# Optimization experiments

Hardware: AMD Instinct MI355X
Metric: run time of the kernel (lower is better)

The kernel has to match this reference:

```python
import jax, jax.numpy as jnp
import numpy as np

B, S, D = 16, 2048, 768  # batch, padded subword length, roberta hidden dim


def setup_inputs() -> dict:
    key = jax.random.key(0)
    k1, k2 = jax.random.split(key)
    robert_embed = jax.random.normal(k1, (B, S, D), dtype=jnp.float32)
    # Non-decreasing per-row segment ids: contiguous runs of equal ids are the
    # subword spans that merge_list would average; singleton runs pass through.
    seg_ids = jnp.sort(jax.random.randint(k2, (B, S), 0, S, dtype=jnp.int32), axis=-1)
    return {"robert_embed": robert_embed, "seg_ids": seg_ids}


def reference(robert_embed, seg_ids):
    # Segment-mean gather/scatter: out[b, w] = mean_{p: seg_ids[b,p]==w} x[b, p]
    b, s, d = robert_embed.shape
    w = s  # output word slots (<= s); empty slots yield zeros
    flat_seg = (seg_ids + (w * jnp.arange(b, dtype=seg_ids.dtype))[:, None]).reshape(-1)
    x_flat = robert_embed.reshape(-1, d)
    sums = jax.ops.segment_sum(x_flat, flat_seg, num_segments=b * w)  # [b*w, d]
    counts = jax.ops.segment_sum(
        jnp.ones((b * s,), dtype=robert_embed.dtype), flat_seg, num_segments=b * w
    )
    out = sums / jnp.maximum(counts, 1)[:, None]
    return out.reshape(b, w, d)
```

## Files before the change

kernel.cpp:

```cpp
#include <hip/hip_runtime.h>

#define BB 16
#define SS 2048
#define DD 768
#define D4 (DD / 4)
#define RB 16
#define RW 4

#define ADD4(A, R) { A.x += R.x; A.y += R.y; A.z += R.z; A.w += R.w; }

#define GLOAD_LDS16_NT(gaddr, laddr)                                           \
    __builtin_amdgcn_global_load_lds(                                          \
        (const __attribute__((address_space(1))) void*)(gaddr),                \
        (__attribute__((address_space(3))) void*)(laddr), 16, 0, 2)

__device__ __forceinline__ void emit_row(float* __restrict__ ob, int v, int vnext,
                                         int c, float4 a0, float4 a1, float4 a2,
                                         int lane) {
    float inv = 1.0f / (float)c;
    a0.x *= inv; a0.y *= inv; a0.z *= inv; a0.w *= inv;
    a1.x *= inv; a1.y *= inv; a1.z *= inv; a1.w *= inv;
    a2.x *= inv; a2.y *= inv; a2.z *= inv; a2.w *= inv;
    float4* op = (float4*)(ob + (size_t)v * DD);
    op[lane]       = a0;
    op[lane + 64]  = a1;
    op[lane + 128] = a2;
    const float4 zz = make_float4(0.f, 0.f, 0.f, 0.f);
    for (int z = v + 1; z < vnext; ++z) {
        float4* zp = (float4*)(ob + (size_t)z * DD);
        zp[lane] = zz; zp[lane + 64] = zz; zp[lane + 128] = zz;
    }
}

__global__ __launch_bounds__(256) void seg_mean_v6(
    const float* __restrict__ x,
    const int*   __restrict__ seg,
    float*       __restrict__ out) {
    __shared__ float lds[RB * DD];
    int lane = threadIdx.x & 63;
    int wv   = threadIdx.x >> 6;
    int p0   = blockIdx.x * RB;
    int b    = p0 >> 11;
    int q0   = p0 & (SS - 1);
    const int*   srow = seg + (b << 11);
    const float* xb   = x   + (size_t)(b << 11) * DD;
    float*       ob   = out + (size_t)(b << 11) * DD;

    {
        const float* gsrc = xb + (size_t)(q0 + wv * RW) * DD + lane * 4;
        float*       ldst = lds + (wv * RW) * DD;
        #pragma unroll
        for (int k = 0; k < RW * 3; ++k) {
            GLOAD_LDS16_NT(gsrc + k * 256, ldst + k * 256);
        }
    }

    int  myv = 0;
    bool startl = false;
    if (lane < RB) {
        int p = q0 + lane;
        myv = srow[p];
        int pv = (p == 0) ? (myv ^ 1) : srow[p - 1];
        startl = (myv != pv);
    }
    unsigned long long smask = __ballot(startl);

    if (q0 == 0 && wv == 0) {
        int first = srow[0];
        const float4 zz = make_float4(0.f, 0.f, 0.f, 0.f);
        for (int z = 0; z < first; ++z) {
            float4* zp = (float4*)(ob + (size_t)z * DD);
            zp[lane] = zz; zp[lane + 64] = zz; zp[lane + 128] = zz;
        }
    }

    __syncthreads();

    unsigned wmask = (unsigned)(smask >> (wv * RW)) & ((1u << RW) - 1);
    while (wmask) {
        int jrel = __builtin_ctz(wmask); wmask &= wmask - 1;
        int j    = wv * RW + jrel;
        int vcur = __shfl(myv, j);

        unsigned long long above = smask >> (j + 1);
        int  e_loc;
        bool tail;
        if (above) { e_loc = j + 1 + (int)__builtin_ctzll(above); tail = false; }
        else       { e_loc = RB;                                  tail = true;  }

        const float4* lp = (const float4*)(lds + (size_t)j * DD);
        float4 a0 = lp[lane], a1 = lp[lane + 64], a2 = lp[lane + 128];
        for (int t = j + 1; t < e_loc; ++t) {
            const float4* q = (const float4*)(lds + (size_t)t * DD);
            float4 r0 = q[lane], r1 = q[lane + 64], r2 = q[lane + 128];
            ADD4(a0, r0); ADD4(a1, r1); ADD4(a2, r2);
        }

        int c, vnext;
        if (!tail) {
            c     = e_loc - j;
            vnext = __shfl(myv, e_loc);
        } else {
            int e = q0 + RB;
            if (e < SS) {
                for (;;) {
                    int idx = e + lane;
                    int vv  = (idx < SS) ? srow[idx] : (vcur ^ 1);
                    unsigned long long m  = __ballot(vv == vcur);
                    unsigned long long nm = ~m;
                    if (nm) { e += (int)__builtin_ctzll(nm); break; }
                    e += 64;
                }
            }
            for (int t = q0 + RB; t < e; ++t) {
                const float4* xn = (const float4*)(xb + (size_t)t * DD);
                float4 r0 = xn[lane], r1 = xn[lane + 64], r2 = xn[lane + 128];
                ADD4(a0, r0); ADD4(a1, r1); ADD4(a2, r2);
            }
            c     = e - (q0 + j);
            vnext = (e < SS) ? srow[e] : SS;
        }
        emit_row(ob, vcur, vnext, c, a0, a1, a2, lane);
    }
}

extern "C" void kernel_launch(void* const* d_in, const int* in_sizes, int n_in,
                              void* d_out, int out_size, void* d_ws, size_t ws_size,
                              hipStream_t stream) {
    const float* x   = (const float*)d_in[0];
    const int*   seg = (const int*)d_in[1];
    float* out = (float*)d_out;

    int nBlocks = (BB * SS) / RB;
    seg_mean_v6<<<nBlocks, 256, 0, stream>>>(x, seg, out);
}
```

Measured before the change: 176.2 us.

## Double-buffer LDS tiles so each block processes several row tiles in a pipeline

Each block now handles four consecutive 8-row tiles instead of one 16-row tile. It prefetches the next tile into a second LDS buffer with async global-to-LDS loads while reducing the current one, using explicit vmcnt waits and barriers. The aim is to overlap load latency with compute and cut the block count. In exchange there are smaller tiles, so more segments spill across the tile tail and trigger global re-reads, plus extra barriers per tile.

```diff
diff --git a/kernel.cpp b/kernel.cpp
--- a/kernel.cpp
+++ b/kernel.cpp
@@ -3,9 +3,11 @@
 #define BB 16
 #define SS 2048
 #define DD 768
-#define D4 (DD / 4)
-#define RB 16
-#define RW 4
+#define RB 8
+#define RW 2
+#define TPB 4
+#define NTILE (BB * SS / RB)
+#define NBLK (NTILE / TPB)
 
 #define ADD4(A, R) { A.x += R.x; A.y += R.y; A.z += R.z; A.w += R.w; }
 
@@ -32,95 +34,114 @@
     }
 }
 
-__global__ __launch_bounds__(256) void seg_mean_v6(
+__global__ __launch_bounds__(256) void seg_mean_v8(
     const float* __restrict__ x,
     const int*   __restrict__ seg,
     float*       __restrict__ out) {
-    __shared__ float lds[RB * DD];
+    __shared__ float lds[2][RB * DD];
     int lane = threadIdx.x & 63;
     int wv   = threadIdx.x >> 6;
-    int p0   = blockIdx.x * RB;
-    int b    = p0 >> 11;
-    int q0   = p0 & (SS - 1);
-    const int*   srow = seg + (b << 11);
-    const float* xb   = x   + (size_t)(b << 11) * DD;
-    float*       ob   = out + (size_t)(b << 11) * DD;
+    int g0   = blockIdx.x * TPB;
 
     {
-        const float* gsrc = xb + (size_t)(q0 + wv * RW) * DD + lane * 4;
-        float*       ldst = lds + (wv * RW) * DD;
+        const float* gsrc = x + (size_t)g0 * (RB * DD) + (wv * RW) * DD + lane * 4;
+        float*       ldst = &lds[0][(wv * RW) * DD];
         #pragma unroll
-        for (int k = 0; k < RW * 3; ++k) {
+        for (int k = 0; k < RW * 3; ++k)
             GLOAD_LDS16_NT(gsrc + k * 256, ldst + k * 256);
-        }
     }
 
-    int  myv = 0;
-    bool startl = false;
-    if (lane < RB) {
-        int p = q0 + lane;
-        myv = srow[p];
-        int pv = (p == 0) ? (myv ^ 1) : srow[p - 1];
-        startl = (myv != pv);
-    }
-    unsigned long long smask = __ballot(startl);
+    #pragma unroll
+    for (int t = 0; t < TPB; ++t) {
+        int g  = g0 + t;
+        int p0 = g * RB;
+        int b  = p0 >> 11;
+        int q0 = p0 & (SS - 1);
 
-    if (q0 == 0 && wv == 0) {
-        int first = srow[0];
-        const float4 zz = make_float4(0.f, 0.f, 0.f, 0.f);
-        for (int z = 0; z < first; ++z) {
-            float4* zp = (float4*)(ob + (size_t)z * DD);
-            zp[lane] = zz; zp[lane + 64] = zz; zp[lane + 128] = zz;
+        if (t + 1 < TPB) {
+            const float* gsrc = x + (size_t)(g + 1) * (RB * DD) + (wv * RW) * DD + lane * 4;
+            float*       ldst = &lds[(t + 1) & 1][(wv * RW) * DD];
+            #pragma unroll
+            for (int k = 0; k < RW * 3; ++k)
+                GLOAD_LDS16_NT(gsrc + k * 256, ldst + k * 256);
+            asm volatile("s_waitcnt vmcnt(6)" ::: "memory");
+        } else {
+            asm volatile("s_waitcnt vmcnt(0)" ::: "memory");
         }
-    }
+        asm volatile("s_barrier" ::: "memory");
 
-    __syncthreads();
+        const float* buf  = lds[t & 1];
+        const int*   srow = seg + (b << 11);
+        const float* xb   = x   + (size_t)(b << 11) * DD;
+        float*       ob   = out + (size_t)(b << 11) * DD;
 
-    unsigned wmask = (unsigned)(smask >> (wv * RW)) & ((1u << RW) - 1);
-    while (wmask) {
-        int jrel = __builtin_ctz(wmask); wmask &= wmask - 1;
-        int j    = wv * RW + jrel;
-        int vcur = __shfl(myv, j);
+        int  myv = 0;
+        bool startl = false;
+        if (lane < RB) {
+            int p = q0 + lane;
+            myv = srow[p];
+            int pv = (p == 0) ? (myv ^ 1) : srow[p - 1];
+            startl = (myv != pv);
+        }
+        unsigned long long smask = __ballot(startl);
 
-        unsigned long long above = smask >> (j + 1);
-        int  e_loc;
-        bool tail;
-        if (above) { e_loc = j + 1 + (int)__builtin_ctzll(above); tail = false; }
-        else       { e_loc = RB;                                  tail = true;  }
-
-        const float4* lp = (const float4*)(lds + (size_t)j * DD);
-        float4 a0 = lp[lane], a1 = lp[lane + 64], a2 = lp[lane + 128];
-        for (int t = j + 1; t < e_loc; ++t) {
-            const float4* q = (const float4*)(lds + (size_t)t * DD);
-            float4 r0 = q[lane], r1 = q[lane + 64], r2 = q[lane + 128];
-            ADD4(a0, r0); ADD4(a1, r1); ADD4(a2, r2);
+        if (q0 == 0 && wv == 0) {
+            int first = srow[0];
+            const float4 zz = make_float4(0.f, 0.f, 0.f, 0.f);
+            for (int z = 0; z < first; ++z) {
+                float4* zp = (float4*)(ob + (size_t)z * DD);
+                zp[lane] = zz; zp[lane + 64] = zz; zp[lane + 128] = zz;
+            }
         }
 
-        int c, vnext;
-        if (!tail) {
-            c     = e_loc - j;
-            vnext = __shfl(myv, e_loc);
-        } else {
-            int e = q0 + RB;
-            if (e < SS) {
-                for (;;) {
-                    int idx = e + lane;
-                    int vv  = (idx < SS) ? srow[idx] : (vcur ^ 1);
-                    unsigned long long m  = __ballot(vv == vcur);
-                    unsigned long long nm = ~m;
-                    if (nm) { e += (int)__builtin_ctzll(nm); break; }
-                    e += 64;
-                }
-            }
-            for (int t = q0 + RB; t < e; ++t) {
-                const float4* xn = (const float4*)(xb + (size_t)t * DD);
-                float4 r0 = xn[lane], r1 = xn[lane + 64], r2 = xn[lane + 128];
+        unsigned wmask = (unsigned)(smask >> (wv * RW)) & ((1u << RW) - 1);
+        while (wmask) {
+            int jrel = __builtin_ctz(wmask); wmask &= wmask - 1;
+            int j    = wv * RW + jrel;
+            int vcur = __shfl(myv, j);
+
+            unsigned long long above = smask >> (j + 1);
+            int  e_loc;
+            bool tail;
+            if (above) { e_loc = j + 1 + (int)__builtin_ctzll(above); tail = false; }
+            else       { e_loc = RB;                                  tail = true;  }
+
+            const float4* lp = (const float4*)(buf + (size_t)j * DD);
+            float4 a0 = lp[lane], a1 = lp[lane + 64], a2 = lp[lane + 128];
+            for (int r = j + 1; r < e_loc; ++r) {
+                const float4* q = (const float4*)(buf + (size_t)r * DD);
+                float4 r0 = q[lane], r1 = q[lane + 64], r2 = q[lane + 128];
                 ADD4(a0, r0); ADD4(a1, r1); ADD4(a2, r2);
             }
-            c     = e - (q0 + j);
-            vnext = (e < SS) ? srow[e] : SS;
+
+            int c, vnext;
+            if (!tail) {
+                c     = e_loc - j;
+                vnext = __shfl(myv, e_loc);
+            } else {
+                int e = q0 + RB;
+                if (e < SS) {
+                    for (;;) {
+                        int idx = e + lane;
+                        int vv  = (idx < SS) ? srow[idx] : (vcur ^ 1);
+                        unsigned long long m  = __ballot(vv == vcur);
+                        unsigned long long nm = ~m;
+                        if (nm) { e += (int)__builtin_ctzll(nm); break; }
+                        e += 64;
+                    }
+                }
+                for (int r = q0 + RB; r < e; ++r) {
+                    const float4* xn = (const float4*)(xb + (size_t)r * DD);
+                    float4 r0 = xn[lane], r1 = xn[lane + 64], r2 = xn[lane + 128];
+                    ADD4(a0, r0); ADD4(a1, r1); ADD4(a2, r2);
+                }
+                c     = e - (q0 + j);
+                vnext = (e < SS) ? srow[e] : SS;
+            }
+            emit_row(ob, vcur, vnext, c, a0, a1, a2, lane);
         }
-        emit_row(ob, vcur, vnext, c, a0, a1, a2, lane);
+
+        asm volatile("s_barrier" ::: "memory");
     }
 }
 
@@ -131,6 +152,5 @@
     const int*   seg = (const int*)d_in[1];
     float* out = (float*)d_out;
 
-    int nBlocks = (BB * SS) / RB;
-    seg_mean_v6<<<nBlocks, 256, 0, stream>>>(x, seg, out);
+    seg_mean_v8<<<NBLK, 256, 0, stream>>>(x, seg, out);
 }
```

Result: slower. 182.4 us (+3.5%).
